# Optimization experiments

Hardware: AMD Instinct MI355X
Metric: run time of the kernel (lower is better)

The kernel has to match this reference:

```python
import jax, jax.numpy as jnp
import numpy as np
from jax import lax

# ---- ConvBlock config (matches init_kwargs) ----
IN_CH, OUT_CH, K, MB = 64, 128, 3, 8
P = OUT_CH // MB            # 16 block-rows
Q = (IN_CH * K * K) // MB   # 72 block-cols (64*9=576, divisible by 8)
BN_EPS = 1e-5
ACT_THRES = 6.0


def setup_inputs() -> dict:
    key = jax.random.key(0)
    k1, k2, k3, k4 = jax.random.split(key, 4)
    x = jax.random.normal(k1, (32, IN_CH, 56, 56), dtype=jnp.float32)
    # block-decomposed MZI weight: [p, q, mb, mb]
    fan_in = IN_CH * K * K
    w_blocks = jax.random.normal(k2, (P, Q, MB, MB), dtype=jnp.float32) * (1.0 / np.sqrt(fan_in))
    gamma = jax.random.uniform(k3, (OUT_CH,), dtype=jnp.float32, minval=0.5, maxval=1.5)
    beta = jax.random.normal(k4, (OUT_CH,), dtype=jnp.float32) * 0.1
    return {"x": x, "w_blocks": w_blocks, "gamma": gamma, "beta": beta}


def _assemble_weight(w_blocks):
    # [p, q, mb, mb] -> dense [p*mb, q*mb] -> crop -> [O, I, K, K]
    p, q, mb, _ = w_blocks.shape
    w = jnp.transpose(w_blocks, (0, 2, 1, 3)).reshape(p * mb, q * mb)
    w = w[:OUT_CH, : IN_CH * K * K]
    return w.reshape(OUT_CH, IN_CH, K, K)


def reference(x, w_blocks, gamma, beta):
    # MZIBlockConv2d, weight mode, w_bit=in_bit=16 => quantizers are identity,
    # photodetect=False => plain real-valued conv with block-assembled weight.
    w = _assemble_weight(w_blocks)
    y = lax.conv_general_dilated(
        x, w,
        window_strides=(1, 1),
        padding=((1, 1), (1, 1)),
        dimension_numbers=("NCHW", "OIHW", "NCHW"),
    )
    # BatchNorm2d in training mode: batch statistics over (N, H, W), biased var
    mean = jnp.mean(y, axis=(0, 2, 3))
    var = jnp.var(y, axis=(0, 2, 3))
    inv = gamma / jnp.sqrt(var + BN_EPS)
    y = (y - mean[None, :, None, None]) * inv[None, :, None, None] + beta[None, :, None, None]
    # ReLUN(6): clipped ReLU
    return jnp.clip(y, 0.0, ACT_THRES)
```

## Files before the change

### kernel.cpp

```cpp
#include <hip/hip_runtime.h>

#define NB    32
#define CIN   64
#define COUT  128
#define HH    56
#define WW    56
#define NPIX  (NB*HH*WW)
#define BN_EPSF 1e-5f

typedef __bf16 bf16x8 __attribute__((ext_vector_type(8)));
typedef float  f32x4  __attribute__((ext_vector_type(4)));
typedef unsigned short u16x8 __attribute__((ext_vector_type(8)));

__global__ void zero_sums(float* g) {
    g[threadIdx.x] = 0.0f;
}

__global__ void assemble_w(const float* __restrict__ wb,
                           __bf16* __restrict__ whi, __bf16* __restrict__ wlo) {
    int idx = blockIdx.x * 256 + threadIdx.x;
    if (idx >= 576 * 128) return;
    int col = idx >> 7, oc = idx & 127;
    int p = oc >> 3, i = oc & 7, q = col >> 3, j = col & 7;
    float v = wb[((p * 72 + q) * 8 + i) * 8 + j];
    int ic = col / 9, tap = col % 9;
    int dst = ((tap * 2 + (ic >> 5)) * 128 + oc) * 32 + (ic & 31);
    __bf16 hi = (__bf16)v;
    whi[dst] = hi;
    wlo[dst] = (__bf16)(v - (float)hi);
}

__global__ __launch_bounds__(256, 2) void conv_mfma(
    const float* __restrict__ x, const __bf16* __restrict__ whi,
    const __bf16* __restrict__ wlo, float* __restrict__ y,
    float* __restrict__ gsum, float* __restrict__ gsq)
{
    __shared__ __bf16 xs_hi[160 * 72];
    __shared__ __bf16 xs_lo[160 * 72];
    __shared__ __bf16 wb_hi[128 * 40];
    __shared__ __bf16 wb_lo[128 * 40];
    __shared__ float  red[256];

    int b = blockIdx.x;
    int n = b / 28, t = b % 28;
    int h0 = (t / 7) * 14, w0 = (t % 7) * 8;
    int tid  = threadIdx.x;
    int lane = tid & 63, wid = tid >> 6;
    int l15 = lane & 15, l4 = lane >> 4;
    int oc0 = wid * 32;

    const float* xn = x + n * CIN * HH * WW;
    for (int idx = tid; idx < 64 * 160; idx += 256) {
        int ic = idx / 160, px = idx - ic * 160;
        int r = px / 10, c = px - r * 10;
        int gh = h0 - 1 + r, gw = w0 - 1 + c;
        float v = 0.0f;
        if ((unsigned)gh < 56u && (unsigned)gw < 56u)
            v = xn[(ic * HH + gh) * WW + gw];
        __bf16 hi = (__bf16)v;
        xs_hi[px * 72 + ic] = hi;
        xs_lo[px * 72 + ic] = (__bf16)(v - (float)hi);
    }

    f32x4 acc[7][2] = {};

    for (int tap = 0; tap < 9; ++tap) {
        int kh = tap / 3, kw = tap - kh * 3;
        for (int half = 0; half < 2; ++half) {
            __syncthreads();
            {
                int base = (tap * 2 + half) * 128 * 32;
                for (int c = tid; c < 512; c += 256) {
                    int oc = c >> 2, part = c & 3;
                    int src = base + oc * 32 + part * 8;
                    int dst = oc * 40 + part * 8;
                    *(u16x8*)&wb_hi[dst] = *(const u16x8*)&whi[src];
                    *(u16x8*)&wb_lo[dst] = *(const u16x8*)&wlo[src];
                }
            }
            __syncthreads();

            int koffA = half * 32 + l4 * 8;
            int koffB = l4 * 8;
            bf16x8 bh0 = *(const bf16x8*)&wb_hi[(oc0 +      l15) * 40 + koffB];
            bf16x8 bh1 = *(const bf16x8*)&wb_hi[(oc0 + 16 + l15) * 40 + koffB];
            bf16x8 bl0 = *(const bf16x8*)&wb_lo[(oc0 +      l15) * 40 + koffB];
            bf16x8 bl1 = *(const bf16x8*)&wb_lo[(oc0 + 16 + l15) * 40 + koffB];

            #pragma unroll
            for (int mt = 0; mt < 7; ++mt) {
                int px = mt * 16 + l15;
                int R  = ((px >> 3) + kh) * 10 + (px & 7) + kw;
                int ae = R * 72 + koffA;
                bf16x8 ah = *(const bf16x8*)&xs_hi[ae];
                bf16x8 al = *(const bf16x8*)&xs_lo[ae];
                acc[mt][0] = __builtin_amdgcn_mfma_f32_16x16x32_bf16(ah, bh0, acc[mt][0], 0, 0, 0);
                acc[mt][1] = __builtin_amdgcn_mfma_f32_16x16x32_bf16(ah, bh1, acc[mt][1], 0, 0, 0);
                acc[mt][0] = __builtin_amdgcn_mfma_f32_16x16x32_bf16(ah, bl0, acc[mt][0], 0, 0, 0);
                acc[mt][1] = __builtin_amdgcn_mfma_f32_16x16x32_bf16(ah, bl1, acc[mt][1], 0, 0, 0);
                acc[mt][0] = __builtin_amdgcn_mfma_f32_16x16x32_bf16(al, bh0, acc[mt][0], 0, 0, 0);
                acc[mt][1] = __builtin_amdgcn_mfma_f32_16x16x32_bf16(al, bh1, acc[mt][1], 0, 0, 0);
            }
        }
    }

    float* yn = y + n * COUT * HH * WW;
    int pyb = l4 >> 1;
    int gwo = w0 + (l4 & 1) * 4;
    #pragma unroll
    for (int mt = 0; mt < 7; ++mt) {
        int gh = h0 + mt * 2 + pyb;
        #pragma unroll
        for (int nt = 0; nt < 2; ++nt) {
            int oc = oc0 + nt * 16 + l15;
            *(float4*)&yn[(oc * HH + gh) * WW + gwo] = *(float4*)&acc[mt][nt];
        }
    }

    #pragma unroll
    for (int nt = 0; nt < 2; ++nt) {
        float s = 0.0f, sq = 0.0f;
        #pragma unroll
        for (int mt = 0; mt < 7; ++mt)
            #pragma unroll
            for (int r = 0; r < 4; ++r) {
                float v = acc[mt][nt][r];
                s += v; sq += v * v;
            }
        s  += __shfl_xor(s, 16, 64);  s  += __shfl_xor(s, 32, 64);
        sq += __shfl_xor(sq, 16, 64); sq += __shfl_xor(sq, 32, 64);
        if (l4 == 0) {
            int oc = oc0 + nt * 16 + l15;
            red[oc] = s; red[128 + oc] = sq;
        }
    }
    __syncthreads();
    if (tid < 128) {
        atomicAdd(&gsum[tid], red[tid]);
        atomicAdd(&gsq[tid],  red[128 + tid]);
    }
}

__global__ void bn_finalize(const float* __restrict__ gsum, const float* __restrict__ gsq,
                            const float* __restrict__ gamma, const float* __restrict__ beta,
                            float* __restrict__ scale, float* __restrict__ shift)
{
    int c = threadIdx.x;
    float mean = gsum[c] * (1.0f / NPIX);
    float var  = gsq[c]  * (1.0f / NPIX) - mean * mean;
    float inv  = gamma[c] / sqrtf(var + BN_EPSF);
    scale[c] = inv;
    shift[c] = beta[c] - mean * inv;
}

__global__ __launch_bounds__(256) void bn_apply(float* __restrict__ y,
        const float* __restrict__ scale, const float* __restrict__ shift)
{
    const int total4 = NB * COUT * HH * WW / 4;
    int idx = blockIdx.x * blockDim.x + threadIdx.x;
    int stride = gridDim.x * blockDim.x;
    for (int i4 = idx; i4 < total4; i4 += stride) {
        int c = (i4 / 784) & 127;
        float sc = scale[c], sh = shift[c];
        float4 v = ((float4*)y)[i4];
        v.x = fminf(fmaxf(fmaf(v.x, sc, sh), 0.0f), 6.0f);
        v.y = fminf(fmaxf(fmaf(v.y, sc, sh), 0.0f), 6.0f);
        v.z = fminf(fmaxf(fmaf(v.z, sc, sh), 0.0f), 6.0f);
        v.w = fminf(fmaxf(fmaf(v.w, sc, sh), 0.0f), 6.0f);
        ((float4*)y)[i4] = v;
    }
}

extern "C" void kernel_launch(void* const* d_in, const int* in_sizes, int n_in,
                              void* d_out, int out_size, void* d_ws, size_t ws_size,
                              hipStream_t stream) {
    const float* x     = (const float*)d_in[0];
    const float* wb    = (const float*)d_in[1];
    const float* gamma = (const float*)d_in[2];
    const float* beta  = (const float*)d_in[3];
    float* y = (float*)d_out;

    __bf16* whi = (__bf16*)d_ws;
    __bf16* wlo = whi + 73728;
    float* stats = (float*)(wlo + 73728);
    float* gsum  = stats;
    float* gsq   = gsum + 128;
    float* scale = gsq + 128;
    float* shift = scale + 128;

    zero_sums<<<1, 256, 0, stream>>>(gsum);
    assemble_w<<<(576 * 128 + 255) / 256, 256, 0, stream>>>(wb, whi, wlo);
    conv_mfma<<<NB * 28, 256, 0, stream>>>(x, whi, wlo, y, gsum, gsq);
    bn_finalize<<<1, COUT, 0, stream>>>(gsum, gsq, gamma, beta, scale, shift);
    bn_apply<<<2048, 256, 0, stream>>>(y, scale, shift);
}
```

Before: 202.7 us.

## Drop weight LDS staging, swizzle input tile, vectorize channel loads, raise occupancy

Weight fragments are now read straight from global memory (through cache) each tap/half, so the per-step LDS copy and its two barriers go away. The input tile is stored without padding, using an XOR swizzle on 8-channel groups to avoid bank conflicts. It is filled with 8-channel vector stores per thread, and the reduction buffer reuses that LDS. Together with the smaller LDS footprint, launch bounds now allow 4 blocks per CU. The cost is that B operands become global-load latency inside the MFMA loop, and register pressure may force spills under the tighter bound.

```diff
diff --git a/kernel.cpp b/kernel.cpp
--- a/kernel.cpp
+++ b/kernel.cpp
@@ -30,16 +30,13 @@
     wlo[dst] = (__bf16)(v - (float)hi);
 }
 
-__global__ __launch_bounds__(256, 2) void conv_mfma(
+__global__ __launch_bounds__(256, 4) void conv_mfma(
     const float* __restrict__ x, const __bf16* __restrict__ whi,
     const __bf16* __restrict__ wlo, float* __restrict__ y,
     float* __restrict__ gsum, float* __restrict__ gsq)
 {
-    __shared__ __bf16 xs_hi[160 * 72];
-    __shared__ __bf16 xs_lo[160 * 72];
-    __shared__ __bf16 wb_hi[128 * 40];
-    __shared__ __bf16 wb_lo[128 * 40];
-    __shared__ float  red[256];
+    __shared__ __bf16 xs_hi[160 * 64];
+    __shared__ __bf16 xs_lo[160 * 64];
 
     int b = blockIdx.x;
     int n = b / 28, t = b % 28;
@@ -50,48 +47,45 @@
     int oc0 = wid * 32;
 
     const float* xn = x + n * CIN * HH * WW;
-    for (int idx = tid; idx < 64 * 160; idx += 256) {
-        int ic = idx / 160, px = idx - ic * 160;
-        int r = px / 10, c = px - r * 10;
-        int gh = h0 - 1 + r, gw = w0 - 1 + c;
-        float v = 0.0f;
-        if ((unsigned)gh < 56u && (unsigned)gw < 56u)
-            v = xn[(ic * HH + gh) * WW + gw];
-        __bf16 hi = (__bf16)v;
-        xs_hi[px * 72 + ic] = hi;
-        xs_lo[px * 72 + ic] = (__bf16)(v - (float)hi);
+    for (int u = tid; u < 1280; u += 256) {
+        int c = u / 160, px = u - c * 160;
+        int r = px / 10, cc = px - r * 10;
+        int gh = h0 - 1 + r, gw = w0 - 1 + cc;
+        bool ok = ((unsigned)gh < 56u) & ((unsigned)gw < 56u);
+        const float* src = xn + (c * 8) * (HH * WW) + gh * WW + gw;
+        bf16x8 hi, lo;
+        #pragma unroll
+        for (int j = 0; j < 8; ++j) {
+            float v = ok ? src[j * HH * WW] : 0.0f;
+            __bf16 h = (__bf16)v;
+            hi[j] = h;
+            lo[j] = (__bf16)(v - (float)h);
+        }
+        int dst = px * 64 + ((c ^ (px & 7)) * 8);
+        *(bf16x8*)&xs_hi[dst] = hi;
+        *(bf16x8*)&xs_lo[dst] = lo;
     }
+    __syncthreads();
 
     f32x4 acc[7][2] = {};
 
     for (int tap = 0; tap < 9; ++tap) {
         int kh = tap / 3, kw = tap - kh * 3;
+        #pragma unroll
         for (int half = 0; half < 2; ++half) {
-            __syncthreads();
-            {
-                int base = (tap * 2 + half) * 128 * 32;
-                for (int c = tid; c < 512; c += 256) {
-                    int oc = c >> 2, part = c & 3;
-                    int src = base + oc * 32 + part * 8;
-                    int dst = oc * 40 + part * 8;
-                    *(u16x8*)&wb_hi[dst] = *(const u16x8*)&whi[src];
-                    *(u16x8*)&wb_lo[dst] = *(const u16x8*)&wlo[src];
-                }
-            }
-            __syncthreads();
-
-            int koffA = half * 32 + l4 * 8;
-            int koffB = l4 * 8;
-            bf16x8 bh0 = *(const bf16x8*)&wb_hi[(oc0 +      l15) * 40 + koffB];
-            bf16x8 bh1 = *(const bf16x8*)&wb_hi[(oc0 + 16 + l15) * 40 + koffB];
-            bf16x8 bl0 = *(const bf16x8*)&wb_lo[(oc0 +      l15) * 40 + koffB];
-            bf16x8 bl1 = *(const bf16x8*)&wb_lo[(oc0 + 16 + l15) * 40 + koffB];
+            const __bf16* bh = whi + ((tap * 2 + half) * 128) * 32;
+            const __bf16* bl = wlo + ((tap * 2 + half) * 128) * 32;
+            bf16x8 bh0 = *(const bf16x8*)&bh[(oc0 +      l15) * 32 + l4 * 8];
+            bf16x8 bh1 = *(const bf16x8*)&bh[(oc0 + 16 + l15) * 32 + l4 * 8];
+            bf16x8 bl0 = *(const bf16x8*)&bl[(oc0 +      l15) * 32 + l4 * 8];
+            bf16x8 bl1 = *(const bf16x8*)&bl[(oc0 + 16 + l15) * 32 + l4 * 8];
+            int cbase = half * 4 + l4;
 
             #pragma unroll
             for (int mt = 0; mt < 7; ++mt) {
                 int px = mt * 16 + l15;
                 int R  = ((px >> 3) + kh) * 10 + (px & 7) + kw;
-                int ae = R * 72 + koffA;
+                int ae = R * 64 + ((cbase ^ (R & 7)) * 8);
                 bf16x8 ah = *(const bf16x8*)&xs_hi[ae];
                 bf16x8 al = *(const bf16x8*)&xs_lo[ae];
                 acc[mt][0] = __builtin_amdgcn_mfma_f32_16x16x32_bf16(ah, bh0, acc[mt][0], 0, 0, 0);
@@ -117,6 +111,8 @@
         }
     }
 
+    float* red = (float*)xs_hi;
+    __syncthreads();
     #pragma unroll
     for (int nt = 0; nt < 2; ++nt) {
         float s = 0.0f, sq = 0.0f;
@@ -182,8 +178,7 @@
 
     __bf16* whi = (__bf16*)d_ws;
     __bf16* wlo = whi + 73728;
-    float* stats = (float*)(wlo + 73728);
-    float* gsum  = stats;
+    float* gsum  = (float*)(wlo + 73728);
     float* gsq   = gsum + 128;
     float* scale = gsq + 128;
     float* shift = scale + 128;
```

Result: faster. 163.2 us (-19.5%).
